# Optimization experiments

Measured on AMD Instinct MI355X. Metric: run time of the kernel, lower is better.

## Reference

```python
import jax, jax.numpy as jnp
import numpy as np

B, S, T, D, K = 8, 500, 30, 5, 10
H, TW, E = 64, 512, 8000


def gru_scan(x, Wi, Wh, bi, bh, lengths=None):
    """Torch-convention GRU. x: [N,T,Din] -> (full [N,T,H], last [N,H]).
    If lengths is given, hidden state freezes past each sequence's length and
    padded steps of `full` are zeroed."""
    N, Tn, _ = x.shape
    Hh = Wh.shape[0]
    xg = jnp.moveaxis(x @ Wi + bi, 1, 0)  # [T,N,3H]

    def step(h, inp):
        xg_t, t = inp
        hg = h @ Wh + bh
        xr, xz, xn = jnp.split(xg_t, 3, axis=-1)
        hr, hz, hn = jnp.split(hg, 3, axis=-1)
        r = jax.nn.sigmoid(xr + hr)
        z = jax.nn.sigmoid(xz + hz)
        n = jnp.tanh(xn + r * hn)
        h_new = (1.0 - z) * n + z * h
        if lengths is not None:
            valid = (t < lengths)[:, None]
            h_new = jnp.where(valid, h_new, h)
            full_t = jnp.where(valid, h_new, 0.0)
        else:
            full_t = h_new
        return h_new, full_t

    h0 = jnp.zeros((N, Hh), x.dtype)
    last, full = jax.lax.scan(step, h0, (xg, jnp.arange(Tn)))
    return jnp.moveaxis(full, 0, 1), last


def layer_norm(x, g, b, eps=1e-5):
    m = jnp.mean(x, axis=-1, keepdims=True)
    v = jnp.var(x, axis=-1, keepdims=True)
    return (x - m) / jnp.sqrt(v + eps) * g + b


def setup_inputs() -> dict:
    key = jax.random.key(0)
    ks = jax.random.split(key, 40)
    p = lambda i, shape: jax.random.normal(ks[i], shape, jnp.float32) * 0.05
    inp = {}
    inp['price'] = jax.random.normal(ks[0], (B, S, T, 3), jnp.float32)
    inp['tweets'] = jax.random.normal(ks[1], (B, S, D, K, TW), jnp.float32)
    inp['tweet_counts'] = jax.random.randint(ks[2], (B, S, D), 0, K + 1, jnp.int32)
    inp['edge_index'] = jax.random.randint(ks[3], (2, E), 0, S, jnp.int32)
    inp['num_edge_type'] = 3
    # price GRU (in=3)
    inp['pg_Wi'] = p(4, (3, 3 * H)); inp['pg_Wh'] = p(5, (H, 3 * H))
    inp['pg_bi'] = p(6, (3 * H,)); inp['pg_bh'] = p(7, (3 * H,))
    # tweet GRU (in=512)
    inp['tg_Wi'] = p(8, (TW, 3 * H)); inp['tg_Wh'] = p(9, (H, 3 * H))
    inp['tg_bi'] = p(10, (3 * H,)); inp['tg_bh'] = p(11, (3 * H,))
    # date GRU (in=64)
    inp['dg_Wi'] = p(12, (H, 3 * H)); inp['dg_Wh'] = p(13, (H, 3 * H))
    inp['dg_bi'] = p(14, (3 * H,)); inp['dg_bh'] = p(15, (3 * H,))
    inp['bil_A'] = p(16, (H, H, H)); inp['bil_b'] = p(17, (H,))
    inp['gnn_W'] = p(18, (H, H)); inp['gnn_b'] = p(19, (H,))
    inp['fc1_W'] = p(20, (2 * H, H)); inp['fc1_b'] = p(21, (H,))
    inp['ln1_g'] = jnp.ones((H,), jnp.float32); inp['ln1_b'] = jnp.zeros((H,), jnp.float32)
    inp['fc2_W'] = p(22, (H, H)); inp['fc2_b'] = p(23, (H,))
    inp['ln2_g'] = jnp.ones((H,), jnp.float32); inp['ln2_b'] = jnp.zeros((H,), jnp.float32)
    inp['mlp_W1'] = p(24, (H, H)); inp['mlp_b1'] = p(25, (H,))
    inp['mlp_W2'] = p(26, (H, 1)); inp['mlp_b2'] = p(27, (1,))
    return inp


def reference(price, tweets, pg_Wi, pg_Wh, pg_bi, pg_bh,
              tg_Wi, tg_Wh, tg_bi, tg_bh, dg_Wi, dg_Wh, dg_bi, dg_bh,
              bil_A, bil_b, gnn_W, gnn_b, fc1_W, fc1_b, ln1_g, ln1_b,
              fc2_W, fc2_b, ln2_g, ln2_b, mlp_W1, mlp_b1, mlp_W2, mlp_b2,
              tweet_counts, edge_index, num_edge_type):
    # NOTE: in the original, attn applies softmax over dim=1 of a [T,1] score,
    # i.e. a size-1 axis, so the weights are identically 1 and the attention
    # context is exactly sum(full, axis=0). We reproduce that exact math.
    # Price branch: GRU over T days for every (window, stock), then masked sum.
    pf, _ = gru_scan(price.reshape(B * S, T, 3), pg_Wi, pg_Wh, pg_bi, pg_bh)
    x = pf.sum(axis=1)  # [B*S, H]

    # Tweet branch: ragged GRU over up to K tweets per (window, stock, date).
    tw = tweets.reshape(B * S * D, K, TW)
    lens = tweet_counts.reshape(B * S * D)
    tf, _ = gru_scan(tw, tg_Wi, tg_Wh, tg_bi, tg_bh, lengths=lens)
    news = tf.sum(axis=1).reshape(B * S, D, H)  # zeros where count==0

    # Date GRU over the D daily news vectors.
    df, _ = gru_scan(news, dg_Wi, dg_Wh, dg_bi, dg_bh)
    text = df.sum(axis=1)  # [B*S, H]

    # Bilinear fusion: out_k = text A_k x + b_k, then tanh.
    comb = jnp.tanh(jnp.einsum('ni,kij,nj->nk', text, bil_A, x) + bil_b)
    ft = comb.reshape(B, S, H)

    # Simple GNN: mean-aggregate neighbor features over edge list, then linear.
    src, dst = edge_index[0], edge_index[1]
    deg = jax.ops.segment_sum(jnp.ones((E,), ft.dtype), dst, num_segments=S)
    denom = jnp.maximum(deg, 1.0)[:, None]
    agg = jax.vmap(lambda m: jax.ops.segment_sum(m, dst, num_segments=S))(ft[:, src, :])
    g = jnp.tanh((agg / denom) @ gnn_W + gnn_b)

    h = jnp.concatenate([ft, g], axis=-1)            # [B,S,2H]
    h = jax.nn.relu(layer_norm(h @ fc1_W + fc1_b, ln1_g, ln1_b))  # dropout: eval
    h = jax.nn.relu(layer_norm(h @ fc2_W + fc2_b, ln2_g, ln2_b))
    h = jax.nn.relu(h @ mlp_W1 + mlp_b1)
    logits = (h @ mlp_W2 + mlp_b2).reshape(B, S)
    return logits
```

## Files before the change

### kernel.cpp

```cpp
#include <hip/hip_runtime.h>
#include <math.h>

#define Bq 8
#define Sq 500
#define Tq 30
#define Dq 5
#define Kq 10
#define Hq 64
#define TWq 512
#define Eq 8000
#define NS (Bq*Sq)
#define NTt (NS*Dq)
#define G3 (3*Hq)
#define TG 4

#define MR 48
#define KC 64
#define XPITCH 72
#define XGP 196
#define NKT (TWq/32)
#define NNT (G3/16)
#define PSEQ 16

typedef __attribute__((ext_vector_type(8))) short short8_t;
typedef __attribute__((ext_vector_type(4))) float float4_t;

__device__ __forceinline__ float fsig(float x) {
    return 1.0f / (1.0f + __expf(-x));
}
__device__ __forceinline__ float ftanh(float x) {
    return 1.0f - 2.0f / (__expf(2.0f * x) + 1.0f);
}

__device__ __forceinline__ float wave_sum64(float v) {
    #pragma unroll
    for (int off = 32; off; off >>= 1) v += __shfl_xor(v, off, 64);
    return v;
}

__device__ __forceinline__ short f32_to_bf16_rn(float f) {
    union { float f; unsigned u; } v; v.f = f;
    unsigned r = v.u + 0x7fffu + ((v.u >> 16) & 1u);
    return (short)(r >> 16);
}
__device__ __forceinline__ float bf16_to_f32(short s) {
    union { unsigned u; float f; } v; v.u = ((unsigned)(unsigned short)s) << 16;
    return v.f;
}

__global__ __launch_bounds__(64)
void wfrag_prep_kernel(const float* __restrict__ Wi,
                       short* __restrict__ Wf_hi, short* __restrict__ Wf_lo) {
    const int kt = blockIdx.x / NNT;
    const int nt = blockIdx.x - kt*NNT;
    const int lane = threadIdx.x;
    const int quad = lane >> 4, l16 = lane & 15;
    short h[8], l[8];
    #pragma unroll
    for (int j = 0; j < 8; j++) {
        int k = kt*32 + quad*8 + j;
        int n = nt*16 + l16;
        float w = Wi[(size_t)k*G3 + n];
        short hi = f32_to_bf16_rn(w);
        short lo = f32_to_bf16_rn(w - bf16_to_f32(hi));
        h[j] = hi; l[j] = lo;
    }
    size_t off = ((size_t)blockIdx.x*64 + lane)*8;
    *(short8_t*)(Wf_hi + off) = *(const short8_t*)h;
    *(short8_t*)(Wf_lo + off) = *(const short8_t*)l;
}

__global__ __launch_bounds__(64)
void bilfrag_prep_kernel(const float* __restrict__ A,
                         short* __restrict__ Bf_hi, short* __restrict__ Bf_lo) {
    const int kt = blockIdx.x >> 2;
    const int nt = blockIdx.x & 3;
    const int lane = threadIdx.x;
    const int quad = lane >> 4, l16 = lane & 15;
    short h[8], l[8];
    #pragma unroll
    for (int j = 0; j < 8; j++) {
        int kidx = kt*32 + quad*8 + j;
        int n = nt*16 + l16;
        float w = A[(size_t)n*4096 + kidx];
        short hi = f32_to_bf16_rn(w);
        h[j] = hi; l[j] = f32_to_bf16_rn(w - bf16_to_f32(hi));
    }
    size_t off = ((size_t)blockIdx.x*64 + lane)*8;
    *(short8_t*)(Bf_hi + off) = *(const short8_t*)h;
    *(short8_t*)(Bf_lo + off) = *(const short8_t*)l;
}

__global__ __launch_bounds__(256)
void price_gru_mfma_kernel(const float* __restrict__ price,
                           const float* __restrict__ Wi,
                           const short* __restrict__ Whf_hi, const short* __restrict__ Whf_lo,
                           const float* __restrict__ bi, const float* __restrict__ bh,
                           float* __restrict__ xout) {
    __shared__ __align__(16) float price_s[PSEQ*90];
    __shared__ __align__(16) short h_hi[PSEQ*72];
    __shared__ __align__(16) short h_lo[PSEQ*72];
    const int tid = threadIdx.x;
    const int n0 = blockIdx.x * PSEQ;
    const int wv = tid >> 6;
    const int lane = tid & 63;
    const int quad = lane >> 4;
    const int l16 = lane & 15;
    const int u = wv*16 + l16;
    for (int i = tid; i < PSEQ*90; i += 256) price_s[i] = price[(size_t)n0*90 + i];
    for (int i = tid; i < PSEQ*72; i += 256) { h_hi[i] = 0; h_lo[i] = 0; }
    float wir[3], wiz[3], win[3];
    #pragma unroll
    for (int k = 0; k < 3; k++) {
        wir[k] = Wi[k*G3 + u];
        wiz[k] = Wi[k*G3 + 64 + u];
        win[k] = Wi[k*G3 + 128 + u];
    }
    const float cbr = bi[u] + bh[u];
    const float cbz = bi[64+u] + bh[64+u];
    const float bin = bi[128+u];
    const float bhn = bh[128+u];
    short8_t bfh[2][3], bfl[2][3];
    #pragma unroll
    for (int kt = 0; kt < 2; kt++)
        #pragma unroll
        for (int g = 0; g < 3; g++) {
            size_t off = (((size_t)kt*NNT + (g*4 + wv))*64 + lane)*8;
            bfh[kt][g] = *(const short8_t*)(Whf_hi + off);
            bfl[kt][g] = *(const short8_t*)(Whf_lo + off);
        }
    float hprev[4] = {0.f,0.f,0.f,0.f}, sum[4] = {0.f,0.f,0.f,0.f};
    __syncthreads();
    for (int t = 0; t < Tq; t++) {
        short8_t ah[2], al[2];
        #pragma unroll
        for (int kt = 0; kt < 2; kt++) {
            int addr = l16*72 + kt*32 + quad*8;
            ah[kt] = *(const short8_t*)&h_hi[addr];
            al[kt] = *(const short8_t*)&h_lo[addr];
        }
        float4_t accr = {0.f,0.f,0.f,0.f}, accz = {0.f,0.f,0.f,0.f}, accn = {0.f,0.f,0.f,0.f};
        #pragma unroll
        for (int kt = 0; kt < 2; kt++) {
            accr = __builtin_amdgcn_mfma_f32_16x16x32_bf16(ah[kt], bfh[kt][0], accr, 0,0,0);
            accr = __builtin_amdgcn_mfma_f32_16x16x32_bf16(ah[kt], bfl[kt][0], accr, 0,0,0);
            accr = __builtin_amdgcn_mfma_f32_16x16x32_bf16(al[kt], bfh[kt][0], accr, 0,0,0);
            accz = __builtin_amdgcn_mfma_f32_16x16x32_bf16(ah[kt], bfh[kt][1], accz, 0,0,0);
            accz = __builtin_amdgcn_mfma_f32_16x16x32_bf16(ah[kt], bfl[kt][1], accz, 0,0,0);
            accz = __builtin_amdgcn_mfma_f32_16x16x32_bf16(al[kt], bfh[kt][1], accz, 0,0,0);
            accn = __builtin_amdgcn_mfma_f32_16x16x32_bf16(ah[kt], bfh[kt][2], accn, 0,0,0);
            accn = __builtin_amdgcn_mfma_f32_16x16x32_bf16(ah[kt], bfl[kt][2], accn, 0,0,0);
            accn = __builtin_amdgcn_mfma_f32_16x16x32_bf16(al[kt], bfh[kt][2], accn, 0,0,0);
        }
        __syncthreads();
        #pragma unroll
        for (int r = 0; r < 4; r++) {
            const int s = quad*4 + r;
            float p0 = price_s[s*90 + t*3 + 0];
            float p1 = price_s[s*90 + t*3 + 1];
            float p2 = price_s[s*90 + t*3 + 2];
            float xr = fmaf(p2, wir[2], fmaf(p1, wir[1], fmaf(p0, wir[0], cbr)));
            float xz = fmaf(p2, wiz[2], fmaf(p1, wiz[1], fmaf(p0, wiz[0], cbz)));
            float xn = fmaf(p2, win[2], fmaf(p1, win[1], fmaf(p0, win[0], bin)));
            float rg = fsig(xr + accr[r]);
            float zg = fsig(xz + accz[r]);
            float ng = ftanh(xn + rg*(accn[r] + bhn));
            float h = (1.0f - zg)*ng + zg*hprev[r];
            hprev[r] = h; sum[r] += h;
            short hh = f32_to_bf16_rn(h);
            h_hi[s*72 + u] = hh;
            h_lo[s*72 + u] = f32_to_bf16_rn(h - bf16_to_f32(hh));
        }
        __syncthreads();
    }
    #pragma unroll
    for (int r = 0; r < 4; r++)
        xout[(size_t)(n0 + quad*4 + r)*Hq + u] = sum[r];
}

__global__ __launch_bounds__(256)
void tweet_gru_kernel(const float* __restrict__ tweets,
                      const int* __restrict__ counts,
                      const short* __restrict__ Wf_hi, const short* __restrict__ Wf_lo,
                      const float* __restrict__ Wh,
                      const float* __restrict__ bi, const float* __restrict__ bh,
                      float* __restrict__ news) {
    __shared__ __align__(16) char smem[MR*XGP*4];
    __shared__ __align__(16) float h_s[TG][Hq];
    __shared__ __align__(16) float hg_s[TG][XGP];
    __shared__ int len_s[TG];
    short* x_hi = (short*)smem;
    short* x_lo = (short*)(smem + MR*XPITCH*2);
    float* xg   = (float*)smem;

    const int tid  = threadIdx.x;
    const int n0   = blockIdx.x * TG;
    const int wave = tid >> 6;
    const int lane = tid & 63;
    const int quad = lane >> 4;
    const int l16  = lane & 15;

    if (tid < TG) {
        int c = counts[n0 + tid];
        len_s[tid] = c < 0 ? 0 : (c > Kq ? Kq : c);
    }

    float4_t acc[3][3];
    #pragma unroll
    for (int a = 0; a < 3; a++)
        #pragma unroll
        for (int b = 0; b < 3; b++)
            acc[a][b] = (float4_t){0.f, 0.f, 0.f, 0.f};

    for (int ch = 0; ch < TWq/KC; ch++) {
        __syncthreads();
        for (int i = tid; i < TG*Kq*(KC/4); i += 256) {
            int row = i >> 4;
            int c4  = i & 15;
            int s   = (row*205) >> 11;
            int t   = row - s*10;
            if (t < len_s[s]) {
                float4 v = *(const float4*)&tweets[(((size_t)(n0+s))*Kq + t)*TWq + ch*KC + c4*4];
                short hh[4], ll[4];
                float f[4] = {v.x, v.y, v.z, v.w};
                #pragma unroll
                for (int j = 0; j < 4; j++) {
                    short hi = f32_to_bf16_rn(f[j]);
                    hh[j] = hi;
                    ll[j] = f32_to_bf16_rn(f[j] - bf16_to_f32(hi));
                }
                *(short4*)&x_hi[row*XPITCH + c4*4] = *(const short4*)hh;
                *(short4*)&x_lo[row*XPITCH + c4*4] = *(const short4*)ll;
            }
        }
        __syncthreads();
        #pragma unroll
        for (int ks = 0; ks < KC/32; ks++) {
            const int kt = ch*(KC/32) + ks;
            short8_t bh_[3], bl_[3];
            #pragma unroll
            for (int ntl = 0; ntl < 3; ntl++) {
                size_t off = (((size_t)kt*NNT + (wave*3 + ntl))*64 + lane)*8;
                bh_[ntl] = *(const short8_t*)(Wf_hi + off);
                bl_[ntl] = *(const short8_t*)(Wf_lo + off);
            }
            short8_t ah_[3], al_[3];
            #pragma unroll
            for (int mt = 0; mt < 3; mt++) {
                int addr = (mt*16 + l16)*XPITCH + ks*32 + quad*8;
                ah_[mt] = *(const short8_t*)&x_hi[addr];
                al_[mt] = *(const short8_t*)&x_lo[addr];
            }
            #pragma unroll
            for (int mt = 0; mt < 3; mt++)
                #pragma unroll
                for (int ntl = 0; ntl < 3; ntl++) {
                    acc[mt][ntl] = __builtin_amdgcn_mfma_f32_16x16x32_bf16(ah_[mt], bh_[ntl], acc[mt][ntl], 0, 0, 0);
                    acc[mt][ntl] = __builtin_amdgcn_mfma_f32_16x16x32_bf16(ah_[mt], bl_[ntl], acc[mt][ntl], 0, 0, 0);
                    acc[mt][ntl] = __builtin_amdgcn_mfma_f32_16x16x32_bf16(al_[mt], bh_[ntl], acc[mt][ntl], 0, 0, 0);
                }
        }
    }
    __syncthreads();
    #pragma unroll
    for (int ntl = 0; ntl < 3; ntl++) {
        const int col = (wave*3 + ntl)*16 + l16;
        const float bic = bi[col];
        #pragma unroll
        for (int mt = 0; mt < 3; mt++) {
            const int row0 = mt*16 + quad*4;
            #pragma unroll
            for (int r = 0; r < 4; r++)
                xg[(row0 + r)*XGP + col] = acc[mt][ntl][r] + bic;
        }
    }
    const int g = tid;
    float w[Hq];
    if (tid < G3) {
        #pragma unroll
        for (int j = 0; j < Hq; j++) w[j] = Wh[(size_t)j*G3 + g];
    }
    const float bhg = (tid < G3) ? bh[g] : 0.0f;
    const int su_s = tid >> 6;
    const int su_u = tid & 63;
    h_s[su_s][su_u] = 0.0f;
    float hreg = 0.0f, sum = 0.0f;
    __syncthreads();
    for (int t = 0; t < Kq; t++) {
        if (tid < G3) {
            #pragma unroll
            for (int s = 0; s < TG; s++) {
                if (t < len_s[s]) {
                    float a0=0.f,a1=0.f,a2=0.f,a3=0.f;
                    #pragma unroll
                    for (int j = 0; j < Hq; j += 4) {
                        float4 hv = *(const float4*)&h_s[s][j];
                        a0 = fmaf(hv.x, w[j+0], a0);
                        a1 = fmaf(hv.y, w[j+1], a1);
                        a2 = fmaf(hv.z, w[j+2], a2);
                        a3 = fmaf(hv.w, w[j+3], a3);
                    }
                    hg_s[s][g] = bhg + ((a0+a1)+(a2+a3));
                }
            }
        }
        __syncthreads();
        if (t < len_s[su_s]) {
            const float* xr = &xg[(su_s*Kq + t)*XGP];
            float r  = fsig(xr[su_u]        + hg_s[su_s][su_u]);
            float z  = fsig(xr[Hq+su_u]     + hg_s[su_s][Hq+su_u]);
            float nn = ftanh(xr[2*Hq+su_u] + r*hg_s[su_s][2*Hq+su_u]);
            hreg = (1.0f - z)*nn + z*hreg;
            sum += hreg;
            h_s[su_s][su_u] = hreg;
        }
        __syncthreads();
    }
    news[(size_t)(n0 + su_s)*Hq + su_u] = sum;
}

__global__ __launch_bounds__(192)
void date_gru_kernel(const float* __restrict__ news,
                     const float* __restrict__ Wi, const float* __restrict__ Wh,
                     const float* __restrict__ bi, const float* __restrict__ bh,
                     float* __restrict__ text) {
    __shared__ __align__(16) float nw_s[Dq*Hq];
    __shared__ __align__(16) float h_s[Hq];
    __shared__ __align__(16) float xg_s[G3];
    __shared__ __align__(16) float hg_s[G3];
    const int n = blockIdx.x;
    const int g = threadIdx.x;
    for (int i = g; i < Dq*Hq; i += 192) nw_s[i] = news[(size_t)n*Dq*Hq + i];
    float wi[Hq], wh[Hq];
    #pragma unroll
    for (int j = 0; j < Hq; j++) { wi[j] = Wi[j*G3+g]; wh[j] = Wh[j*G3+g]; }
    const float big = bi[g], bhg = bh[g];
    if (g < Hq) h_s[g] = 0.0f;
    float hreg = 0.0f, sum = 0.0f;
    __syncthreads();
    for (int t = 0; t < Dq; t++) {
        float a0=0.f,a1=0.f,a2=0.f,a3=0.f, b0=0.f,b1=0.f,b2=0.f,b3=0.f;
        #pragma unroll
        for (int j = 0; j < Hq; j += 4) {
            float4 nv = *(const float4*)&nw_s[t*Hq + j];
            float4 hv = *(const float4*)&h_s[j];
            a0 = fmaf(nv.x, wi[j+0], a0);
            a1 = fmaf(nv.y, wi[j+1], a1);
            a2 = fmaf(nv.z, wi[j+2], a2);
            a3 = fmaf(nv.w, wi[j+3], a3);
            b0 = fmaf(hv.x, wh[j+0], b0);
            b1 = fmaf(hv.y, wh[j+1], b1);
            b2 = fmaf(hv.z, wh[j+2], b2);
            b3 = fmaf(hv.w, wh[j+3], b3);
        }
        xg_s[g] = big + ((a0+a1)+(a2+a3));
        hg_s[g] = bhg + ((b0+b1)+(b2+b3));
        __syncthreads();
        if (g < Hq) {
            float r  = fsig(xg_s[g]      + hg_s[g]);
            float z  = fsig(xg_s[Hq+g]   + hg_s[Hq+g]);
            float nn = ftanh(xg_s[2*Hq+g] + r*hg_s[2*Hq+g]);
            hreg = (1.0f - z)*nn + z*hreg;
            sum += hreg;
            h_s[g] = hreg;
        }
        __syncthreads();
    }
    if (g < Hq) text[(size_t)n*Hq + g] = sum;
}

#define TP 68
#define XP 72
__global__ __launch_bounds__(256)
void bilinear_mfma_kernel(const float* __restrict__ text, const float* __restrict__ x,
                          const short* __restrict__ Bf_hi, const short* __restrict__ Bf_lo,
                          const float* __restrict__ bb, float* __restrict__ ft) {
    __shared__ __align__(16) float t_s[16*TP];
    __shared__ __align__(16) float x_s[16*XP];
    const int tid = threadIdx.x;
    const int n0 = blockIdx.x * 16;
    const int wv = tid >> 6, lane = tid & 63, quad = lane >> 4, l16 = lane & 15;
    for (int i = tid; i < 16*64; i += 256) {
        int r = i >> 6, c = i & 63;
        t_s[r*TP + c] = text[(size_t)(n0 + r)*Hq + c];
        x_s[r*XP + c] = x[(size_t)(n0 + r)*Hq + c];
    }
    float4_t acc = {0.f,0.f,0.f,0.f};
    __syncthreads();
    for (int kt = 0; kt < 128; kt++) {
        const int i  = kt >> 1;
        const int j0 = (kt & 1)*32 + quad*8;
        size_t boff = (((size_t)kt*4 + wv)*64 + lane)*8;
        short8_t bh_ = *(const short8_t*)(Bf_hi + boff);
        short8_t bl_ = *(const short8_t*)(Bf_lo + boff);
        float ti = t_s[l16*TP + i];
        float xv[8];
        *(float4*)&xv[0] = *(const float4*)&x_s[l16*XP + j0];
        *(float4*)&xv[4] = *(const float4*)&x_s[l16*XP + j0 + 4];
        short ph[8], pl[8];
        #pragma unroll
        for (int jj = 0; jj < 8; jj++) {
            float p = ti * xv[jj];
            short hi = f32_to_bf16_rn(p);
            ph[jj] = hi;
            pl[jj] = f32_to_bf16_rn(p - bf16_to_f32(hi));
        }
        short8_t ah = *(const short8_t*)ph;
        short8_t al = *(const short8_t*)pl;
        acc = __builtin_amdgcn_mfma_f32_16x16x32_bf16(ah, bh_, acc, 0,0,0);
        acc = __builtin_amdgcn_mfma_f32_16x16x32_bf16(ah, bl_, acc, 0,0,0);
        acc = __builtin_amdgcn_mfma_f32_16x16x32_bf16(al, bh_, acc, 0,0,0);
    }
    const int col = wv*16 + l16;
    const float bk = bb[col];
    #pragma unroll
    for (int r = 0; r < 4; r++) {
        int n = quad*4 + r;
        ft[(size_t)(n0 + n)*Hq + col] = ftanh(acc[r] + bk);
    }
}

__global__ void deg_kernel(const int* __restrict__ ei, float* __restrict__ deg) {
    int e = blockIdx.x*256 + threadIdx.x;
    if (e < Eq) atomicAdd(&deg[ei[Eq + e]], 1.0f);
}

__global__ void agg_kernel(const int* __restrict__ ei, const float* __restrict__ ft,
                           float* __restrict__ agg) {
    int gid = blockIdx.x*256 + threadIdx.x;
    int e = gid >> 6;
    int u = gid & 63;
    if (e < Eq) {
        int src = ei[e], dst = ei[Eq + e];
        #pragma unroll
        for (int b = 0; b < Bq; b++) {
            atomicAdd(&agg[((size_t)(b*Sq + dst))*Hq + u],
                      ft[((size_t)(b*Sq + src))*Hq + u]);
        }
    }
}

__global__ __launch_bounds__(64)
void head_kernel(const float* __restrict__ ft, const float* __restrict__ agg,
                 const float* __restrict__ deg,
                 const float* __restrict__ gnn_W, const float* __restrict__ gnn_b,
                 const float* __restrict__ fc1_W, const float* __restrict__ fc1_b,
                 const float* __restrict__ ln1_g, const float* __restrict__ ln1_b,
                 const float* __restrict__ fc2_W, const float* __restrict__ fc2_b,
                 const float* __restrict__ ln2_g, const float* __restrict__ ln2_b,
                 const float* __restrict__ mlp_W1, const float* __restrict__ mlp_b1,
                 const float* __restrict__ mlp_W2, const float* __restrict__ mlp_b2,
                 float* __restrict__ out) {
    __shared__ __align__(16) float a_s[Hq];
    __shared__ __align__(16) float in_s[2*Hq];
    __shared__ __align__(16) float t_s[Hq];
    const int n = blockIdx.x;
    const int s = n % Sq;
    const int u = threadIdx.x;
    const float denom = fmaxf(deg[s], 1.0f);
    a_s[u]  = agg[(size_t)n*Hq + u] / denom;
    in_s[u] = ft[(size_t)n*Hq + u];
    __syncthreads();
    {
        float a0=0.f,a1=0.f,a2=0.f,a3=0.f;
        #pragma unroll
        for (int j = 0; j < Hq; j += 4) {
            a0 = fmaf(a_s[j+0], gnn_W[(j+0)*Hq + u], a0);
            a1 = fmaf(a_s[j+1], gnn_W[(j+1)*Hq + u], a1);
            a2 = fmaf(a_s[j+2], gnn_W[(j+2)*Hq + u], a2);
            a3 = fmaf(a_s[j+3], gnn_W[(j+3)*Hq + u], a3);
        }
        in_s[Hq+u] = ftanh(gnn_b[u] + ((a0+a1)+(a2+a3)));
    }
    __syncthreads();
    float v;
    {
        float a0=0.f,a1=0.f,a2=0.f,a3=0.f;
        #pragma unroll
        for (int j = 0; j < 2*Hq; j += 4) {
            a0 = fmaf(in_s[j+0], fc1_W[(j+0)*Hq + u], a0);
            a1 = fmaf(in_s[j+1], fc1_W[(j+1)*Hq + u], a1);
            a2 = fmaf(in_s[j+2], fc1_W[(j+2)*Hq + u], a2);
            a3 = fmaf(in_s[j+3], fc1_W[(j+3)*Hq + u], a3);
        }
        v = fc1_b[u] + ((a0+a1)+(a2+a3));
        float m = wave_sum64(v) * (1.0f/Hq);
        float d = v - m;
        float var = wave_sum64(d*d) * (1.0f/Hq);
        v = fmaxf(d * rsqrtf(var + 1e-5f) * ln1_g[u] + ln1_b[u], 0.0f);
    }
    t_s[u] = v;
    __syncthreads();
    {
        float a0=0.f,a1=0.f,a2=0.f,a3=0.f;
        #pragma unroll
        for (int j = 0; j < Hq; j += 4) {
            a0 = fmaf(t_s[j+0], fc2_W[(j+0)*Hq + u], a0);
            a1 = fmaf(t_s[j+1], fc2_W[(j+1)*Hq + u], a1);
            a2 = fmaf(t_s[j+2], fc2_W[(j+2)*Hq + u], a2);
            a3 = fmaf(t_s[j+3], fc2_W[(j+3)*Hq + u], a3);
        }
        v = fc2_b[u] + ((a0+a1)+(a2+a3));
        float m = wave_sum64(v) * (1.0f/Hq);
        float d = v - m;
        float var = wave_sum64(d*d) * (1.0f/Hq);
        v = fmaxf(d * rsqrtf(var + 1e-5f) * ln2_g[u] + ln2_b[u], 0.0f);
    }
    __syncthreads();
    a_s[u] = v;
    __syncthreads();
    {
        float a0=0.f,a1=0.f,a2=0.f,a3=0.f;
        #pragma unroll
        for (int j = 0; j < Hq; j += 4) {
            a0 = fmaf(a_s[j+0], mlp_W1[(j+0)*Hq + u], a0);
            a1 = fmaf(a_s[j+1], mlp_W1[(j+1)*Hq + u], a1);
            a2 = fmaf(a_s[j+2], mlp_W1[(j+2)*Hq + u], a2);
            a3 = fmaf(a_s[j+3], mlp_W1[(j+3)*Hq + u], a3);
        }
        v = fmaxf(mlp_b1[u] + ((a0+a1)+(a2+a3)), 0.0f);
    }
    float p = wave_sum64(v * mlp_W2[u]);
    if (u == 0) out[n] = p + mlp_b2[0];
}

extern "C" void kernel_launch(void* const* d_in, const int* in_sizes, int n_in,
                              void* d_out, int out_size, void* d_ws, size_t ws_size,
                              hipStream_t stream) {
    (void)in_sizes; (void)n_in; (void)out_size; (void)ws_size;
    const float* price  = (const float*)d_in[0];
    const float* tweets = (const float*)d_in[1];
    const int*   counts = (const int*)d_in[2];
    const int*   ei     = (const int*)d_in[3];
    const float* pg_Wi = (const float*)d_in[5];
    const float* pg_Wh = (const float*)d_in[6];
    const float* pg_bi = (const float*)d_in[7];
    const float* pg_bh = (const float*)d_in[8];
    const float* tg_Wi = (const float*)d_in[9];
    const float* tg_Wh = (const float*)d_in[10];
    const float* tg_bi = (const float*)d_in[11];
    const float* tg_bh = (const float*)d_in[12];
    const float* dg_Wi = (const float*)d_in[13];
    const float* dg_Wh = (const float*)d_in[14];
    const float* dg_bi = (const float*)d_in[15];
    const float* dg_bh = (const float*)d_in[16];
    const float* bil_A = (const float*)d_in[17];
    const float* bil_b = (const float*)d_in[18];
    const float* gnn_W = (const float*)d_in[19];
    const float* gnn_b = (const float*)d_in[20];
    const float* fc1_W = (const float*)d_in[21];
    const float* fc1_b = (const float*)d_in[22];
    const float* ln1_g = (const float*)d_in[23];
    const float* ln1_b = (const float*)d_in[24];
    const float* fc2_W = (const float*)d_in[25];
    const float* fc2_b = (const float*)d_in[26];
    const float* ln2_g = (const float*)d_in[27];
    const float* ln2_b = (const float*)d_in[28];
    const float* mlp_W1 = (const float*)d_in[29];
    const float* mlp_b1 = (const float*)d_in[30];
    const float* mlp_W2 = (const float*)d_in[31];
    const float* mlp_b2 = (const float*)d_in[32];

    float* ws      = (float*)d_ws;
    float* x_price = ws;
    float* news    = ws + 256000;
    float* text    = ws + 1536000;
    float* ft      = ws + 1792000;
    float* agg     = ws + 2048000;
    float* deg     = ws + 2304000;
    short* Wf_hi   = (short*)(ws + 2304512);
    short* Wf_lo   = Wf_hi  + 98304;
    short* Whp_hi  = Wf_lo  + 98304;
    short* Whp_lo  = Whp_hi + 12288;
    short* Bf_hi   = Whp_lo + 12288;
    short* Bf_lo   = Bf_hi  + 262144;

    hipMemsetAsync(agg, 0, (256000 + 512)*sizeof(float), stream);

    wfrag_prep_kernel<<<NKT*NNT, 64, 0, stream>>>(tg_Wi, Wf_hi, Wf_lo);
    wfrag_prep_kernel<<<2*NNT, 64, 0, stream>>>(pg_Wh, Whp_hi, Whp_lo);
    bilfrag_prep_kernel<<<128*4, 64, 0, stream>>>(bil_A, Bf_hi, Bf_lo);

    price_gru_mfma_kernel<<<NS/PSEQ, 256, 0, stream>>>(price, pg_Wi, Whp_hi, Whp_lo,
                                                       pg_bi, pg_bh, x_price);
    tweet_gru_kernel<<<NTt/TG, 256, 0, stream>>>(tweets, counts, Wf_hi, Wf_lo,
                                                 tg_Wh, tg_bi, tg_bh, news);
    date_gru_kernel<<<NS, 192, 0, stream>>>(news, dg_Wi, dg_Wh, dg_bi, dg_bh, text);
    bilinear_mfma_kernel<<<NS/16, 256, 0, stream>>>(text, x_price, Bf_hi, Bf_lo, bil_b, ft);
    deg_kernel<<<(Eq+255)/256, 256, 0, stream>>>(ei, deg);
    agg_kernel<<<(Eq*Hq)/256, 256, 0, stream>>>(ei, ft, agg);
    head_kernel<<<NS, 64, 0, stream>>>(ft, agg, deg,
                                       gnn_W, gnn_b, fc1_W, fc1_b, ln1_g, ln1_b,
                                       fc2_W, fc2_b, ln2_g, ln2_b,
                                       mlp_W1, mlp_b1, mlp_W2, mlp_b2,
                                       (float*)d_out);
}
```

Measured before the change: 945.2 us.

## Double-buffer tweet staging with register prefetch and rebalance GRU gate work across waves

```diff
diff --git a/kernel.cpp b/kernel.cpp
--- a/kernel.cpp
+++ b/kernel.cpp
@@ -21,6 +21,10 @@
 #define NKT (TWq/32)
 #define NNT (G3/16)
 #define PSEQ 16
+
+#define XROWS 40
+#define STG_PLANE (MR*XPITCH)
+#define STG_BUF  (2*STG_PLANE)
 
 typedef __attribute__((ext_vector_type(8))) short short8_t;
 typedef __attribute__((ext_vector_type(4))) float float4_t;
@@ -178,20 +182,20 @@
         xout[(size_t)(n0 + quad*4 + r)*Hq + u] = sum[r];
 }
 
-__global__ __launch_bounds__(256)
+__global__ __launch_bounds__(256, 4)
 void tweet_gru_kernel(const float* __restrict__ tweets,
                       const int* __restrict__ counts,
                       const short* __restrict__ Wf_hi, const short* __restrict__ Wf_lo,
                       const float* __restrict__ Wh,
                       const float* __restrict__ bi, const float* __restrict__ bh,
                       float* __restrict__ news) {
-    __shared__ __align__(16) char smem[MR*XGP*4];
+    __shared__ __align__(16) char smem[XROWS*XGP*4];
     __shared__ __align__(16) float h_s[TG][Hq];
-    __shared__ __align__(16) float hg_s[TG][XGP];
+    __shared__ __align__(16) float hg_s[TG][G3];
     __shared__ int len_s[TG];
-    short* x_hi = (short*)smem;
-    short* x_lo = (short*)(smem + MR*XPITCH*2);
-    float* xg   = (float*)smem;
+    __shared__ int tmax_s;
+    short* stg = (short*)smem;
+    float* xg  = (float*)smem;
 
     const int tid  = threadIdx.x;
     const int n0   = blockIdx.x * TG;
@@ -204,6 +208,29 @@
         int c = counts[n0 + tid];
         len_s[tid] = c < 0 ? 0 : (c > Kq ? Kq : c);
     }
+    __syncthreads();
+    if (tid == 0) {
+        int m01 = len_s[0] > len_s[1] ? len_s[0] : len_s[1];
+        int m23 = len_s[2] > len_s[3] ? len_s[2] : len_s[3];
+        tmax_s = m01 > m23 ? m01 : m23;
+    }
+
+    const float* gp[3];
+    int lofs[3];
+    bool val[3];
+    #pragma unroll
+    for (int j = 0; j < 3; j++) {
+        const int ii = tid + j*256;
+        const bool ok = ii < TG*Kq*(KC/4);
+        const int i = ok ? ii : 0;
+        const int row = i >> 4;
+        const int c4  = i & 15;
+        const int s   = (row*205) >> 11;
+        const int t   = row - s*10;
+        val[j]  = ok && (t < len_s[s]);
+        gp[j]   = tweets + (((size_t)(n0+s))*Kq + t)*TWq + c4*4;
+        lofs[j] = row*XPITCH + c4*4;
+    }
 
     float4_t acc[3][3];
     #pragma unroll
@@ -212,28 +239,32 @@
         for (int b = 0; b < 3; b++)
             acc[a][b] = (float4_t){0.f, 0.f, 0.f, 0.f};
 
+    #pragma unroll
+    for (int j = 0; j < 3; j++) if (val[j]) {
+        float4 v = *(const float4*)(gp[j]);
+        float f[4] = {v.x, v.y, v.z, v.w};
+        short hh[4], ll[4];
+        #pragma unroll
+        for (int q = 0; q < 4; q++) {
+            short hi = f32_to_bf16_rn(f[q]);
+            hh[q] = hi;
+            ll[q] = f32_to_bf16_rn(f[q] - bf16_to_f32(hi));
+        }
+        *(short4*)&stg[lofs[j]]             = *(const short4*)hh;
+        *(short4*)&stg[STG_PLANE + lofs[j]] = *(const short4*)ll;
+    }
+    __syncthreads();
+
     for (int ch = 0; ch < TWq/KC; ch++) {
-        __syncthreads();
-        for (int i = tid; i < TG*Kq*(KC/4); i += 256) {
-            int row = i >> 4;
-            int c4  = i & 15;
-            int s   = (row*205) >> 11;
-            int t   = row - s*10;
-            if (t < len_s[s]) {
-                float4 v = *(const float4*)&tweets[(((size_t)(n0+s))*Kq + t)*TWq + ch*KC + c4*4];
-                short hh[4], ll[4];
-                float f[4] = {v.x, v.y, v.z, v.w};
-                #pragma unroll
-                for (int j = 0; j < 4; j++) {
-                    short hi = f32_to_bf16_rn(f[j]);
-                    hh[j] = hi;
-                    ll[j] = f32_to_bf16_rn(f[j] - bf16_to_f32(hi));
-                }
-                *(short4*)&x_hi[row*XPITCH + c4*4] = *(const short4*)hh;
-                *(short4*)&x_lo[row*XPITCH + c4*4] = *(const short4*)ll;
-            }
-        }
-        __syncthreads();
+        const int cur = ch & 1;
+        float4 v[3];
+        if (ch < TWq/KC - 1) {
+            #pragma unroll
+            for (int j = 0; j < 3; j++) if (val[j])
+                v[j] = *(const float4*)(gp[j] + (ch+1)*KC);
+        }
+        const short* xh = stg + cur*STG_BUF;
+        const short* xl = xh + STG_PLANE;
         #pragma unroll
         for (int ks = 0; ks < KC/32; ks++) {
             const int kt = ch*(KC/32) + ks;
@@ -248,8 +279,8 @@
             #pragma unroll
             for (int mt = 0; mt < 3; mt++) {
                 int addr = (mt*16 + l16)*XPITCH + ks*32 + quad*8;
-                ah_[mt] = *(const short8_t*)&x_hi[addr];
-                al_[mt] = *(const short8_t*)&x_lo[addr];
+                ah_[mt] = *(const short8_t*)&xh[addr];
+                al_[mt] = *(const short8_t*)&xl[addr];
             }
             #pragma unroll
             for (int mt = 0; mt < 3; mt++)
@@ -260,8 +291,26 @@
                     acc[mt][ntl] = __builtin_amdgcn_mfma_f32_16x16x32_bf16(al_[mt], bh_[ntl], acc[mt][ntl], 0, 0, 0);
                 }
         }
-    }
-    __syncthreads();
+        if (ch < TWq/KC - 1) {
+            short* yh = stg + (cur^1)*STG_BUF;
+            short* yl = yh + STG_PLANE;
+            #pragma unroll
+            for (int j = 0; j < 3; j++) if (val[j]) {
+                float f[4] = {v[j].x, v[j].y, v[j].z, v[j].w};
+                short hh[4], ll[4];
+                #pragma unroll
+                for (int q = 0; q < 4; q++) {
+                    short hi = f32_to_bf16_rn(f[q]);
+                    hh[q] = hi;
+                    ll[q] = f32_to_bf16_rn(f[q] - bf16_to_f32(hi));
+                }
+                *(short4*)&yh[lofs[j]] = *(const short4*)hh;
+                *(short4*)&yl[lofs[j]] = *(const short4*)ll;
+            }
+        }
+        __syncthreads();
+    }
+
     #pragma unroll
     for (int ntl = 0; ntl < 3; ntl++) {
         const int col = (wave*3 + ntl)*16 + l16;
@@ -269,25 +318,29 @@
         #pragma unroll
         for (int mt = 0; mt < 3; mt++) {
             const int row0 = mt*16 + quad*4;
-            #pragma unroll
-            for (int r = 0; r < 4; r++)
-                xg[(row0 + r)*XGP + col] = acc[mt][ntl][r] + bic;
-        }
-    }
-    const int g = tid;
+            if (row0 < XROWS) {
+                #pragma unroll
+                for (int r = 0; r < 4; r++)
+                    xg[(row0 + r)*XGP + col] = acc[mt][ntl][r] + bic;
+            }
+        }
+    }
+    const int gcol = wave*48 + (lane & 63);
+    const bool gact = lane < 48;
     float w[Hq];
-    if (tid < G3) {
-        #pragma unroll
-        for (int j = 0; j < Hq; j++) w[j] = Wh[(size_t)j*G3 + g];
-    }
-    const float bhg = (tid < G3) ? bh[g] : 0.0f;
-    const int su_s = tid >> 6;
-    const int su_u = tid & 63;
+    if (gact) {
+        #pragma unroll
+        for (int j = 0; j < Hq; j++) w[j] = Wh[(size_t)j*G3 + gcol];
+    }
+    const float bhg = gact ? bh[gcol] : 0.0f;
+    const int su_s = wave;
+    const int su_u = lane;
     h_s[su_s][su_u] = 0.0f;
     float hreg = 0.0f, sum = 0.0f;
     __syncthreads();
-    for (int t = 0; t < Kq; t++) {
-        if (tid < G3) {
+    const int tmax = tmax_s;
+    for (int t = 0; t < tmax; t++) {
+        if (gact) {
             #pragma unroll
             for (int s = 0; s < TG; s++) {
                 if (t < len_s[s]) {
@@ -300,7 +353,7 @@
                         a2 = fmaf(hv.z, w[j+2], a2);
                         a3 = fmaf(hv.w, w[j+3], a3);
                     }
-                    hg_s[s][g] = bhg + ((a0+a1)+(a2+a3));
+                    hg_s[s][gcol] = bhg + ((a0+a1)+(a2+a3));
                 }
             }
         }
```

New measurement: 879.5 us. 7.0% less time.
